# Optimization experiments

Hardware: AMD Instinct MI355X
Metric: run time of the kernel (lower is better)

## Reference

```python
import jax, jax.numpy as jnp
import numpy as np

N, E, F, H, L, G = 100000, 1600000, 32, 128, 4, 64


def gru_cell(m, h, w_ih, b_ih, w_hh, b_hh):
    # torch.nn.GRUCell math; gate order: r, z, n
    gi = m @ w_ih.T + b_ih          # [N, 3H]
    gh = h @ w_hh.T + b_hh          # [N, 3H]
    i_r, i_z, i_n = jnp.split(gi, 3, axis=-1)
    h_r, h_z, h_n = jnp.split(gh, 3, axis=-1)
    r = jax.nn.sigmoid(i_r + h_r)
    z = jax.nn.sigmoid(i_z + h_z)
    n = jnp.tanh(i_n + r * h_n)
    return (1.0 - z) * n + z * h


def setup_inputs() -> dict:
    key = jax.random.key(0)
    ks = jax.random.split(key, 12)
    s = 0.05
    return {
        "x": jax.random.normal(ks[0], (N, F), jnp.float32),
        "edge_index": jax.random.randint(ks[1], (2, E), 0, N, jnp.int64),
        "batch": jnp.sort(jax.random.randint(ks[2], (N,), 0, G, jnp.int64)),
        "num_graphs": G,
        "W0": jax.random.normal(ks[3], (H, F), jnp.float32) * s,
        "conv_w": jax.random.normal(ks[4], (L, H, H), jnp.float32) * s,
        "w_ih": jax.random.normal(ks[5], (3 * H, H), jnp.float32) * s,
        "b_ih": jax.random.normal(ks[6], (3 * H,), jnp.float32) * s,
        "w_hh": jax.random.normal(ks[7], (3 * H, H), jnp.float32) * s,
        "b_hh": jax.random.normal(ks[8], (3 * H,), jnp.float32) * s,
        "lin1_w": jax.random.normal(ks[9], (1, H), jnp.float32) * s,
        "lin1_b": jax.random.normal(ks[10], (1,), jnp.float32) * s,
    }


def reference(x, edge_index, batch, num_graphs, W0, conv_w, w_ih, b_ih, w_hh, b_hh, lin1_w, lin1_b):
    n_nodes = x.shape[0]
    # lin0 (no bias) + sigmoid embedding
    x_embed = jax.nn.sigmoid(x @ W0.T)                     # [N, H]

    src, dst = edge_index[0], edge_index[1]
    h = x_embed
    # GatedGraphConv: per layer, transform -> scatter-add over edges -> GRU update
    for l in range(conv_w.shape[0]):
        m = h @ conv_w[l]                                   # [N, H]
        agg = jax.ops.segment_sum(m[src], dst, num_segments=n_nodes)  # [N, H]
        h = gru_cell(agg, h, w_ih, b_ih, w_hh, b_hh)

    h = jax.nn.relu(h)
    out = h @ lin1_w.T + lin1_b                             # [N, 1]
    uncorrected = out

    # per-graph mean subtraction (scatter_mean + gather), same math as the loop
    sums = jax.ops.segment_sum(out, batch, num_segments=num_graphs)   # [G, 1]
    counts = jax.ops.segment_sum(jnp.ones((n_nodes, 1), out.dtype), batch, num_segments=num_graphs)
    mean_all = sums / jnp.maximum(counts, 1.0)
    corrected = out - mean_all[batch]

    return corrected.squeeze(1), x_embed, uncorrected.squeeze(1)
```

## Files before the change

### kernel.cpp

```cpp
#include <hip/hip_runtime.h>
#include <hip/hip_bf16.h>

#define HDIM 128
#define FDIM 32
#define GGR  64
#define SCAN_CHUNK 2048
#define FILL_CHUNK 1024
#define FILL_WIN 16

typedef __attribute__((ext_vector_type(8))) short bf16x8;
typedef __attribute__((ext_vector_type(4))) float f32x4;

__device__ __forceinline__ float fsig(float x) {
  return __builtin_amdgcn_rcpf(1.f + __expf(-x));
}
__device__ __forceinline__ float ftanh(float x) {
  return 1.f - 2.f * __builtin_amdgcn_rcpf(1.f + __expf(2.f * x));
}

__device__ __forceinline__ bf16x8 pack_bf16x8(float4 a, float4 b) {
  union { bf16x8 v; __hip_bfloat162 h[4]; } u;
  u.h[0] = __float22bfloat162_rn(make_float2(a.x, a.y));
  u.h[1] = __float22bfloat162_rn(make_float2(a.z, a.w));
  u.h[2] = __float22bfloat162_rn(make_float2(b.x, b.y));
  u.h[3] = __float22bfloat162_rn(make_float2(b.z, b.w));
  return u.v;
}

__device__ __forceinline__ int ablk(int kb, int m) {
  return (kb << 6) + (m & 56) + ((m ^ kb) & 7);
}

__device__ __forceinline__ void stage64(const unsigned short* __restrict__ g,
                                        short* __restrict__ s, int n0, int N, int t) {
#pragma unroll
  for (int r = 0; r < 2; ++r) {
    int idx = r * 512 + t;
    int m = idx >> 4, c8 = idx & 15;
    int gn = n0 + m;
    uint4 v = make_uint4(0u, 0u, 0u, 0u);
    if (gn < N) v = *(const uint4*)(g + (size_t)gn * HDIM + c8 * 8);
    *(uint4*)(s + ablk(c8, m) * 8) = v;
  }
}

__global__ __launch_bounds__(256) void k_embed_hist(const float* __restrict__ x,
                                                    const unsigned short* __restrict__ W0b,
                                                    unsigned short* __restrict__ hb,
                                                    float* __restrict__ xemb,
                                                    const unsigned short* __restrict__ convT0,
                                                    unsigned short* __restrict__ m_out,
                                                    int N,
                                                    const int* __restrict__ dst,
                                                    int* __restrict__ deg,
                                                    unsigned short* __restrict__ rank,
                                                    long long E, int histBlocks) {
  __shared__ short sE[16 * 64 * 8];
  if ((int)blockIdx.x < histBlocks) {
    long long e = (long long)blockIdx.x * 256 + threadIdx.x;
    if (e < E) {
      int old = atomicAdd(&deg[dst[e]], 1);
      rank[e] = (unsigned short)old;
    }
    return;
  }
  int bid = blockIdx.x - histBlocks;
  int t = threadIdx.x;
  int w = t >> 6, l = t & 63;
  int lm = l & 15, lq = l >> 4;
  int n0 = bid * 64;
  int j0 = w * 32;
  bf16x8 b0 = *(const bf16x8*)(W0b + (size_t)(j0 + lm) * FDIM + lq * 8);
  bf16x8 b1 = *(const bf16x8*)(W0b + (size_t)(j0 + 16 + lm) * FDIM + lq * 8);
  f32x4 acc0[4], acc1[4];
#pragma unroll
  for (int i = 0; i < 4; ++i) { acc0[i] = (f32x4){0.f,0.f,0.f,0.f}; acc1[i] = (f32x4){0.f,0.f,0.f,0.f}; }
#pragma unroll
  for (int tt = 0; tt < 4; ++tt) {
    int rg = n0 + tt * 16 + lm;
    bf16x8 a = (bf16x8){0,0,0,0,0,0,0,0};
    if (rg < N) {
      const float4* xr = (const float4*)x + (size_t)rg * 8 + lq * 2;
      a = pack_bf16x8(xr[0], xr[1]);
    }
    acc0[tt] = __builtin_amdgcn_mfma_f32_16x16x32_bf16(a, b0, acc0[tt], 0, 0, 0);
    acc1[tt] = __builtin_amdgcn_mfma_f32_16x16x32_bf16(a, b1, acc1[tt], 0, 0, 0);
  }
#pragma unroll
  for (int g = 0; g < 2; ++g) {
    int j = j0 + g * 16 + lm;
#pragma unroll
    for (int tt = 0; tt < 4; ++tt)
#pragma unroll
      for (int r = 0; r < 4; ++r) {
        int m = tt * 16 + lq * 4 + r;
        int node = n0 + m;
        float v = g ? acc1[tt][r] : acc0[tt][r];
        float e = fsig(v);
        __hip_bfloat16 eb = __float2bfloat16(e);
        ((__hip_bfloat16*)sE)[ablk(j >> 3, m) * 8 + (j & 7)] = eb;
        if (node < N) {
          size_t off = (size_t)node * HDIM + j;
          xemb[off] = e;
          ((__hip_bfloat16*)hb)[off] = eb;
        }
      }
  }
  __syncthreads();
#pragma unroll
  for (int g = 0; g < 2; ++g) {
    int jg = j0 + g * 16;
    f32x4 macc[4];
#pragma unroll
    for (int i = 0; i < 4; ++i) macc[i] = (f32x4){0.f,0.f,0.f,0.f};
#pragma unroll
    for (int ks = 0; ks < 4; ++ks) {
      bf16x8 b = *(const bf16x8*)(convT0 + (size_t)(jg + lm) * HDIM + ks * 32 + lq * 8);
      int kb = ks * 4 + lq;
#pragma unroll
      for (int tt = 0; tt < 4; ++tt) {
        bf16x8 a = *(const bf16x8*)(sE + ablk(kb, tt * 16 + lm) * 8);
        macc[tt] = __builtin_amdgcn_mfma_f32_16x16x32_bf16(a, b, macc[tt], 0, 0, 0);
      }
    }
    int j = jg + lm;
#pragma unroll
    for (int tt = 0; tt < 4; ++tt)
#pragma unroll
      for (int r = 0; r < 4; ++r) {
        int node = n0 + tt * 16 + lq * 4 + r;
        if (node < N)
          ((__hip_bfloat16*)m_out)[(size_t)node * HDIM + j] = __float2bfloat16(macc[tt][r]);
      }
  }
}

__global__ __launch_bounds__(256) void k_prep_w(const float* __restrict__ w_ih,
                                                const float* __restrict__ w_hh,
                                                const float* __restrict__ conv_w,
                                                const float* __restrict__ W0,
                                                unsigned short* __restrict__ wIb,
                                                unsigned short* __restrict__ wHb,
                                                unsigned short* __restrict__ convTb,
                                                unsigned short* __restrict__ W0b,
                                                int L) {
  int i = blockIdx.x * 256 + threadIdx.x;
  if (i < HDIM * FDIM) ((__hip_bfloat16*)W0b)[i] = __float2bfloat16(W0[i]);
  if (i < 384 * HDIM) {
    ((__hip_bfloat16*)wIb)[i] = __float2bfloat16(w_ih[i]);
    ((__hip_bfloat16*)wHb)[i] = __float2bfloat16(w_hh[i]);
  }
  int total = L * HDIM * HDIM;
  if (i < total) {
    int l = i >> 14, rem = i & 16383, j = rem >> 7, k = rem & 127;
    ((__hip_bfloat16*)convTb)[i] = __float2bfloat16(conv_w[(l << 14) + (k << 7) + j]);
  }
}

__global__ __launch_bounds__(256) void k_block_sum(const int* __restrict__ deg,
                                                   int* __restrict__ bsum, int N) {
  int base = blockIdx.x * SCAN_CHUNK + threadIdx.x * 8;
  int s = 0;
#pragma unroll
  for (int u = 0; u < 8; ++u) { int i = base + u; if (i < N) s += deg[i]; }
#pragma unroll
  for (int o = 32; o; o >>= 1) s += __shfl_down(s, o, 64);
  __shared__ int wsum[4];
  if ((threadIdx.x & 63) == 0) wsum[threadIdx.x >> 6] = s;
  __syncthreads();
  if (threadIdx.x == 0) bsum[blockIdx.x] = wsum[0] + wsum[1] + wsum[2] + wsum[3];
}

__global__ void k_scan_bsums(int* __restrict__ bsum, int nb) {
  if (blockIdx.x == 0 && threadIdx.x == 0) {
    int run = 0;
    for (int i = 0; i < nb; ++i) { int v = bsum[i]; bsum[i] = run; run += v; }
  }
}

__global__ __launch_bounds__(256) void k_scan_chunks(const int* __restrict__ deg,
                                                     const int* __restrict__ bsum,
                                                     int* __restrict__ rowstart,
                                                     int N, int Etot) {
  __shared__ int ts[256];
  int base = blockIdx.x * SCAN_CHUNK + threadIdx.x * 8;
  int loc[8]; int s = 0;
#pragma unroll
  for (int u = 0; u < 8; ++u) {
    int i = base + u; loc[u] = s;
    s += (i < N) ? deg[i] : 0;
  }
  ts[threadIdx.x] = s;
  __syncthreads();
  for (int o = 1; o < 256; o <<= 1) {
    int v = (threadIdx.x >= o) ? ts[threadIdx.x - o] : 0;
    __syncthreads();
    ts[threadIdx.x] += v;
    __syncthreads();
  }
  int texcl = (threadIdx.x ? ts[threadIdx.x - 1] : 0) + bsum[blockIdx.x];
#pragma unroll
  for (int u = 0; u < 8; ++u) {
    int i = base + u;
    if (i < N) rowstart[i] = texcl + loc[u];
  }
  if (blockIdx.x == 0 && threadIdx.x == 0) rowstart[N] = Etot;
}

__global__ __launch_bounds__(256) void k_csr_fill_win(const int* __restrict__ src,
                                                      const int* __restrict__ dst,
                                                      const unsigned short* __restrict__ rank,
                                                      const int* __restrict__ rowstart,
                                                      int* __restrict__ csr,
                                                      long long E, int N) {
  __shared__ int sd[FILL_CHUNK];
  __shared__ int ss[FILL_CHUNK];
  __shared__ unsigned short sr[FILL_CHUNK];
  long long base = (long long)blockIdx.x * FILL_CHUNK;
  int cnt = (int)((E - base < FILL_CHUNK) ? (E - base) : FILL_CHUNK);
  for (int i = threadIdx.x; i < cnt; i += 256) {
    sd[i] = dst[base + i];
    ss[i] = src[base + i];
    sr[i] = rank[base + i];
  }
  __syncthreads();
  int nw = (N + FILL_WIN - 1) / FILL_WIN;
#pragma unroll 1
  for (int w = 0; w < FILL_WIN; ++w) {
    int lo = w * nw, hi = lo + nw;
    for (int i = threadIdx.x; i < cnt; i += 256) {
      int d = sd[i];
      if (d >= lo && d < hi)
        csr[rowstart[d] + sr[i]] = ss[i];
    }
    __syncthreads();
  }
}

__global__ __launch_bounds__(256) void k_gather(const int* __restrict__ csr,
                                                const int* __restrict__ rowstart,
                                                const unsigned short* __restrict__ m,
                                                unsigned short* __restrict__ agg, int N) {
  int wv = threadIdx.x >> 6, l = threadIdx.x & 63;
  int n = blockIdx.x * 4 + wv;
  if (n >= N) return;
  int eq = l >> 3;
  int jb = l & 7;
  int beg = rowstart[n], end = rowstart[n + 1];
  float acc[16];
#pragma unroll
  for (int i = 0; i < 16; ++i) acc[i] = 0.f;
  for (int e0 = beg; e0 < end; e0 += 8) {
    int e = e0 + eq;
    uint4 v0 = make_uint4(0u, 0u, 0u, 0u);
    uint4 v1 = make_uint4(0u, 0u, 0u, 0u);
    if (e < end) {
      int s = csr[e];
      const uint4* row = (const uint4*)(m + (size_t)s * HDIM + jb * 16);
      v0 = row[0];
      v1 = row[1];
    }
    acc[0]  += __uint_as_float(v0.x << 16);
    acc[1]  += __uint_as_float(v0.x & 0xffff0000u);
    acc[2]  += __uint_as_float(v0.y << 16);
    acc[3]  += __uint_as_float(v0.y & 0xffff0000u);
    acc[4]  += __uint_as_float(v0.z << 16);
    acc[5]  += __uint_as_float(v0.z & 0xffff0000u);
    acc[6]  += __uint_as_float(v0.w << 16);
    acc[7]  += __uint_as_float(v0.w & 0xffff0000u);
    acc[8]  += __uint_as_float(v1.x << 16);
    acc[9]  += __uint_as_float(v1.x & 0xffff0000u);
    acc[10] += __uint_as_float(v1.y << 16);
    acc[11] += __uint_as_float(v1.y & 0xffff0000u);
    acc[12] += __uint_as_float(v1.z << 16);
    acc[13] += __uint_as_float(v1.z & 0xffff0000u);
    acc[14] += __uint_as_float(v1.w << 16);
    acc[15] += __uint_as_float(v1.w & 0xffff0000u);
  }
#pragma unroll
  for (int i = 0; i < 16; ++i) {
    acc[i] += __shfl_xor(acc[i], 8, 64);
    acc[i] += __shfl_xor(acc[i], 16, 64);
    acc[i] += __shfl_xor(acc[i], 32, 64);
  }
  if (eq == 0) {
    union { uint4 v[2]; __hip_bfloat162 h[8]; } o;
#pragma unroll
    for (int i = 0; i < 8; ++i)
      o.h[i] = __float22bfloat162_rn(make_float2(acc[2 * i], acc[2 * i + 1]));
    uint4* dstp = (uint4*)(agg + (size_t)n * HDIM + jb * 16);
    dstp[0] = o.v[0];
    dstp[1] = o.v[1];
  }
}

__global__ __launch_bounds__(512, 4) void k_gru_mfma(const unsigned short* __restrict__ aggb,
                                                  const unsigned short* __restrict__ hb,
                                                  const unsigned short* __restrict__ wI,
                                                  const unsigned short* __restrict__ wH,
                                                  const float* __restrict__ b_ih,
                                                  const float* __restrict__ b_hh,
                                                  unsigned short* __restrict__ hnewb,
                                                  const unsigned short* __restrict__ wT,
                                                  unsigned short* __restrict__ m_out,
                                                  int N) {
  __shared__ short sAg[16 * 64 * 8];
  __shared__ short sH[16 * 64 * 8];
  int t = threadIdx.x;
  int n0 = blockIdx.x * 64;
  stage64(aggb, sAg, n0, N, t);
  stage64(hb, sH, n0, N, t);
  int w = t >> 6, l = t & 63;
  int j0 = w * 16;
  int lm = l & 15, lq = l >> 4;
  int j = j0 + lm;
  float bir = b_ih[j], biz = b_ih[j + 128], bin = b_ih[j + 256];
  float bhr = b_hh[j], bhz = b_hh[j + 128], bhn = b_hh[j + 256];
  __syncthreads();
  f32x4 aR[4], aZ[4], aNi[4], aNh[4];
#pragma unroll
  for (int i = 0; i < 4; ++i) {
    aR[i] = (f32x4){0.f,0.f,0.f,0.f}; aZ[i] = (f32x4){0.f,0.f,0.f,0.f};
    aNi[i] = (f32x4){0.f,0.f,0.f,0.f}; aNh[i] = (f32x4){0.f,0.f,0.f,0.f};
  }
#pragma unroll
  for (int ks = 0; ks < 4; ++ks) {
    size_t rI = (size_t)(j0 + lm) * HDIM + ks * 32 + lq * 8;
    bf16x8 bIr = *(const bf16x8*)(wI + rI);
    bf16x8 bIz = *(const bf16x8*)(wI + rI + 128 * HDIM);
    bf16x8 bIn = *(const bf16x8*)(wI + rI + 256 * HDIM);
    bf16x8 bHr = *(const bf16x8*)(wH + rI);
    bf16x8 bHz = *(const bf16x8*)(wH + rI + 128 * HDIM);
    bf16x8 bHn = *(const bf16x8*)(wH + rI + 256 * HDIM);
    int kb = ks * 4 + lq;
#pragma unroll
    for (int tt = 0; tt < 4; ++tt) {
      bf16x8 a = *(const bf16x8*)(sAg + ablk(kb, tt * 16 + lm) * 8);
      bf16x8 h = *(const bf16x8*)(sH + ablk(kb, tt * 16 + lm) * 8);
      aR[tt] = __builtin_amdgcn_mfma_f32_16x16x32_bf16(a, bIr, aR[tt], 0, 0, 0);
      aR[tt] = __builtin_amdgcn_mfma_f32_16x16x32_bf16(h, bHr, aR[tt], 0, 0, 0);
      aZ[tt] = __builtin_amdgcn_mfma_f32_16x16x32_bf16(a, bIz, aZ[tt], 0, 0, 0);
      aZ[tt] = __builtin_amdgcn_mfma_f32_16x16x32_bf16(h, bHz, aZ[tt], 0, 0, 0);
      aNi[tt] = __builtin_amdgcn_mfma_f32_16x16x32_bf16(a, bIn, aNi[tt], 0, 0, 0);
      aNh[tt] = __builtin_amdgcn_mfma_f32_16x16x32_bf16(h, bHn, aNh[tt], 0, 0, 0);
    }
  }
  __syncthreads();
#pragma unroll
  for (int tt = 0; tt < 4; ++tt)
#pragma unroll
    for (int r = 0; r < 4; ++r) {
      int m = tt * 16 + lq * 4 + r;
      int node = n0 + m;
      float hp = __bfloat162float(((const __hip_bfloat16*)sH)[ablk(j >> 3, m) * 8 + (j & 7)]);
      float rg = fsig(aR[tt][r] + bir + bhr);
      float zg = fsig(aZ[tt][r] + biz + bhz);
      float nv = aNi[tt][r] + bin + rg * (aNh[tt][r] + bhn);
      float th = ftanh(nv);
      float hn = (1.f - zg) * th + zg * hp;
      __hip_bfloat16 hnb = __float2bfloat16(hn);
      ((__hip_bfloat16*)sAg)[ablk(j >> 3, m) * 8 + (j & 7)] = hnb;
      if (node < N)
        ((__hip_bfloat16*)hnewb)[(size_t)node * HDIM + j] = hnb;
    }
  if (wT) {
    __syncthreads();
    f32x4 macc[4];
#pragma unroll
    for (int i = 0; i < 4; ++i) macc[i] = (f32x4){0.f,0.f,0.f,0.f};
#pragma unroll
    for (int ks = 0; ks < 4; ++ks) {
      bf16x8 b = *(const bf16x8*)(wT + (size_t)(j0 + lm) * HDIM + ks * 32 + lq * 8);
      int kb = ks * 4 + lq;
#pragma unroll
      for (int tt = 0; tt < 4; ++tt) {
        bf16x8 a = *(const bf16x8*)(sAg + ablk(kb, tt * 16 + lm) * 8);
        macc[tt] = __builtin_amdgcn_mfma_f32_16x16x32_bf16(a, b, macc[tt], 0, 0, 0);
      }
    }
#pragma unroll
    for (int tt = 0; tt < 4; ++tt)
#pragma unroll
      for (int r = 0; r < 4; ++r) {
        int node = n0 + tt * 16 + lq * 4 + r;
        if (node < N)
          ((__hip_bfloat16*)m_out)[(size_t)node * HDIM + j] = __float2bfloat16(macc[tt][r]);
      }
  }
}

__global__ __launch_bounds__(256) void k_readout(const unsigned short* __restrict__ h,
                                                 const float* __restrict__ w1,
                                                 const float* __restrict__ b1,
                                                 float* __restrict__ out_raw,
                                                 float* __restrict__ uncorrected,
                                                 int N) {
  int wave = threadIdx.x >> 6;
  int lane = threadIdx.x & 63;
  int n = blockIdx.x * 4 + wave;
  if (n >= N) return;
  float h0 = __bfloat162float(((const __hip_bfloat16*)h)[(size_t)n * HDIM + lane]);
  float h1 = __bfloat162float(((const __hip_bfloat16*)h)[(size_t)n * HDIM + 64 + lane]);
  float v = fmaxf(h0, 0.f) * w1[lane] + fmaxf(h1, 0.f) * w1[64 + lane];
#pragma unroll
  for (int o = 32; o > 0; o >>= 1) v += __shfl_down(v, o, 64);
  if (lane == 0) {
    float o = v + b1[0];
    out_raw[n] = o;
    uncorrected[n] = o;
  }
}

__global__ __launch_bounds__(256) void k_graph_reduce(const float* __restrict__ out_raw,
                                                      const int* __restrict__ batch,
                                                      float* __restrict__ gsum,
                                                      float* __restrict__ gcnt,
                                                      int N) {
  __shared__ float ls[GGR], lc[GGR];
  int t = threadIdx.x;
  if (t < GGR) { ls[t] = 0.f; lc[t] = 0.f; }
  __syncthreads();
  for (int n = blockIdx.x * 256 + t; n < N; n += gridDim.x * 256) {
    int g = batch[n];
    atomicAdd(&ls[g], out_raw[n]);
    atomicAdd(&lc[g], 1.f);
  }
  __syncthreads();
  if (t < GGR) {
    unsafeAtomicAdd(&gsum[t], ls[t]);
    unsafeAtomicAdd(&gcnt[t], lc[t]);
  }
}

__global__ __launch_bounds__(256) void k_correct(const float* __restrict__ out_raw,
                                                 const int* __restrict__ batch,
                                                 const float* __restrict__ gsum,
                                                 const float* __restrict__ gcnt,
                                                 float* __restrict__ corrected, int N) {
  int n = blockIdx.x * 256 + threadIdx.x;
  if (n < N) {
    int g = batch[n];
    corrected[n] = out_raw[n] - gsum[g] / fmaxf(gcnt[g], 1.f);
  }
}

extern "C" void kernel_launch(void* const* d_in, const int* in_sizes, int n_in,
                              void* d_out, int out_size, void* d_ws, size_t ws_size,
                              hipStream_t stream) {
  const float* x      = (const float*)d_in[0];
  const int*   ei     = (const int*)d_in[1];
  const int*   batch  = (const int*)d_in[2];
  const float* W0     = (const float*)d_in[4];
  const float* conv_w = (const float*)d_in[5];
  const float* w_ih   = (const float*)d_in[6];
  const float* b_ih   = (const float*)d_in[7];
  const float* w_hh   = (const float*)d_in[8];
  const float* b_hh   = (const float*)d_in[9];
  const float* lin1_w = (const float*)d_in[10];
  const float* lin1_b = (const float*)d_in[11];

  int N = in_sizes[0] / FDIM;
  long long E = in_sizes[1] / 2;
  int L = in_sizes[5] / (HDIM * HDIM);

  const int* src = ei;
  const int* dstv = ei + E;

  float* out_corrected = (float*)d_out;
  float* out_xemb = out_corrected + N;
  float* out_unc  = out_xemb + (size_t)N * HDIM;

  char* p = (char*)d_ws;
  unsigned short* x0 = (unsigned short*)p; p += (size_t)N * HDIM * 2;
  unsigned short* x1 = (unsigned short*)p; p += (size_t)N * HDIM * 2;
  unsigned short* x2 = (unsigned short*)p; p += (size_t)N * HDIM * 2;
  float* out_raw = (float*)p;        p += (size_t)((N + 3) & ~3) * 4;
  float* gsum = (float*)p;           p += GGR * 4;
  float* gcnt = (float*)p;           p += GGR * 4;
  int* deg = (int*)p;                p += (size_t)((N + 3) & ~3) * 4;
  int* rowstart = (int*)p;           p += (size_t)(N + 4) * 4;
  int nb = (N + SCAN_CHUNK - 1) / SCAN_CHUNK;
  int* bsum = (int*)p;               p += (size_t)((nb + 63) & ~63) * 4;
  int* csr = (int*)p;                p += (size_t)E * 4;
  unsigned short* rankb = (unsigned short*)p;  p += (size_t)((E + 3) & ~3) * 2;
  unsigned short* wIb = (unsigned short*)p;    p += 384 * HDIM * 2;
  unsigned short* wHb = (unsigned short*)p;    p += 384 * HDIM * 2;
  unsigned short* convTb = (unsigned short*)p; p += (size_t)L * HDIM * HDIM * 2;
  unsigned short* W0b = (unsigned short*)p;

  int prep_total = (384 * HDIM > L * HDIM * HDIM) ? 384 * HDIM : L * HDIM * HDIM;
  k_prep_w<<<(prep_total + 255) / 256, 256, 0, stream>>>(w_ih, w_hh, conv_w, W0, wIb, wHb, convTb, W0b, L);

  hipMemsetAsync(deg, 0, (size_t)N * sizeof(int), stream);

  int nblk = (N + 63) / 64;
  int histBlocks = (int)((E + 255) / 256);
  k_embed_hist<<<histBlocks + nblk, 256, 0, stream>>>(x, W0b, x0, out_xemb, convTb, x1, N,
                                                      dstv, deg, rankb, E, histBlocks);

  k_block_sum<<<nb, 256, 0, stream>>>(deg, bsum, N);
  k_scan_bsums<<<1, 64, 0, stream>>>(bsum, nb);
  k_scan_chunks<<<nb, 256, 0, stream>>>(deg, bsum, rowstart, N, (int)E);
  k_csr_fill_win<<<(int)((E + FILL_CHUNK - 1) / FILL_CHUNK), 256, 0, stream>>>(
      src, dstv, rankb, rowstart, csr, E, N);

  unsigned short* Hb = x0;
  unsigned short* Mb = x1;
  for (int l = 0; l < L; ++l) {
    k_gather<<<(N + 3) / 4, 256, 0, stream>>>(csr, rowstart, Mb, x2, N);
    const unsigned short* wTn = (l + 1 < L) ? (convTb + (size_t)(l + 1) * HDIM * HDIM) : nullptr;
    k_gru_mfma<<<nblk, 512, 0, stream>>>(x2, Hb, wIb, wHb, b_ih, b_hh, Mb, wTn, Hb, N);
    unsigned short* tmp = Hb; Hb = Mb; Mb = tmp;
  }

  hipMemsetAsync(gsum, 0, 2 * GGR * sizeof(float), stream);
  k_readout<<<(N + 3) / 4, 256, 0, stream>>>(Hb, lin1_w, lin1_b, out_raw, out_unc, N);
  k_graph_reduce<<<256, 256, 0, stream>>>(out_raw, batch, gsum, gcnt, N);
  k_correct<<<(N + 255) / 256, 256, 0, stream>>>(out_raw, batch, gsum, gcnt, out_corrected, N);
}
```

Baseline: 740.7 us.

## Fuse CSR neighbor gather into GRU MFMA kernel via shared memory

Removes the separate gather kernel. Each GRU block now builds the aggregated messages for its 64 nodes directly in shared memory, one wave handling 8 nodes in turn. This drops the global write and re-read of the agg buffer plus one launch per layer. Buffers rotate across three arrays so the message input and the outputs never alias. The cost is lower parallelism for the latency-bound gather: 8 waves per block process nodes serially with fewer blocks in flight, and the GRU's occupancy limits now also apply to the gather.

```diff
diff --git a/kernel.cpp b/kernel.cpp
--- a/kernel.cpp
+++ b/kernel.cpp
@@ -237,64 +237,9 @@
   }
 }
 
-__global__ __launch_bounds__(256) void k_gather(const int* __restrict__ csr,
-                                                const int* __restrict__ rowstart,
-                                                const unsigned short* __restrict__ m,
-                                                unsigned short* __restrict__ agg, int N) {
-  int wv = threadIdx.x >> 6, l = threadIdx.x & 63;
-  int n = blockIdx.x * 4 + wv;
-  if (n >= N) return;
-  int eq = l >> 3;
-  int jb = l & 7;
-  int beg = rowstart[n], end = rowstart[n + 1];
-  float acc[16];
-#pragma unroll
-  for (int i = 0; i < 16; ++i) acc[i] = 0.f;
-  for (int e0 = beg; e0 < end; e0 += 8) {
-    int e = e0 + eq;
-    uint4 v0 = make_uint4(0u, 0u, 0u, 0u);
-    uint4 v1 = make_uint4(0u, 0u, 0u, 0u);
-    if (e < end) {
-      int s = csr[e];
-      const uint4* row = (const uint4*)(m + (size_t)s * HDIM + jb * 16);
-      v0 = row[0];
-      v1 = row[1];
-    }
-    acc[0]  += __uint_as_float(v0.x << 16);
-    acc[1]  += __uint_as_float(v0.x & 0xffff0000u);
-    acc[2]  += __uint_as_float(v0.y << 16);
-    acc[3]  += __uint_as_float(v0.y & 0xffff0000u);
-    acc[4]  += __uint_as_float(v0.z << 16);
-    acc[5]  += __uint_as_float(v0.z & 0xffff0000u);
-    acc[6]  += __uint_as_float(v0.w << 16);
-    acc[7]  += __uint_as_float(v0.w & 0xffff0000u);
-    acc[8]  += __uint_as_float(v1.x << 16);
-    acc[9]  += __uint_as_float(v1.x & 0xffff0000u);
-    acc[10] += __uint_as_float(v1.y << 16);
-    acc[11] += __uint_as_float(v1.y & 0xffff0000u);
-    acc[12] += __uint_as_float(v1.z << 16);
-    acc[13] += __uint_as_float(v1.z & 0xffff0000u);
-    acc[14] += __uint_as_float(v1.w << 16);
-    acc[15] += __uint_as_float(v1.w & 0xffff0000u);
-  }
-#pragma unroll
-  for (int i = 0; i < 16; ++i) {
-    acc[i] += __shfl_xor(acc[i], 8, 64);
-    acc[i] += __shfl_xor(acc[i], 16, 64);
-    acc[i] += __shfl_xor(acc[i], 32, 64);
-  }
-  if (eq == 0) {
-    union { uint4 v[2]; __hip_bfloat162 h[8]; } o;
-#pragma unroll
-    for (int i = 0; i < 8; ++i)
-      o.h[i] = __float22bfloat162_rn(make_float2(acc[2 * i], acc[2 * i + 1]));
-    uint4* dstp = (uint4*)(agg + (size_t)n * HDIM + jb * 16);
-    dstp[0] = o.v[0];
-    dstp[1] = o.v[1];
-  }
-}
-
-__global__ __launch_bounds__(512, 4) void k_gru_mfma(const unsigned short* __restrict__ aggb,
+__global__ __launch_bounds__(512, 4) void k_gru_mfma(const int* __restrict__ csr,
+                                                  const int* __restrict__ rowstart,
+                                                  const unsigned short* __restrict__ mb,
                                                   const unsigned short* __restrict__ hb,
                                                   const unsigned short* __restrict__ wI,
                                                   const unsigned short* __restrict__ wH,
@@ -308,7 +253,6 @@
   __shared__ short sH[16 * 64 * 8];
   int t = threadIdx.x;
   int n0 = blockIdx.x * 64;
-  stage64(aggb, sAg, n0, N, t);
   stage64(hb, sH, n0, N, t);
   int w = t >> 6, l = t & 63;
   int j0 = w * 16;
@@ -316,6 +260,62 @@
   int j = j0 + lm;
   float bir = b_ih[j], biz = b_ih[j + 128], bin = b_ih[j + 256];
   float bhr = b_hh[j], bhz = b_hh[j + 128], bhn = b_hh[j + 256];
+  {
+    int eq = l >> 3;
+    int jb = l & 7;
+#pragma unroll 1
+    for (int i = 0; i < 8; ++i) {
+      int m = w * 8 + i;
+      int n = n0 + m;
+      float acc[16];
+#pragma unroll
+      for (int k = 0; k < 16; ++k) acc[k] = 0.f;
+      if (n < N) {
+        int beg = rowstart[n], end = rowstart[n + 1];
+        for (int e0 = beg; e0 < end; e0 += 8) {
+          int e = e0 + eq;
+          uint4 v0 = make_uint4(0u, 0u, 0u, 0u);
+          uint4 v1 = make_uint4(0u, 0u, 0u, 0u);
+          if (e < end) {
+            int s = csr[e];
+            const uint4* row = (const uint4*)(mb + (size_t)s * HDIM + jb * 16);
+            v0 = row[0];
+            v1 = row[1];
+          }
+          acc[0]  += __uint_as_float(v0.x << 16);
+          acc[1]  += __uint_as_float(v0.x & 0xffff0000u);
+          acc[2]  += __uint_as_float(v0.y << 16);
+          acc[3]  += __uint_as_float(v0.y & 0xffff0000u);
+          acc[4]  += __uint_as_float(v0.z << 16);
+          acc[5]  += __uint_as_float(v0.z & 0xffff0000u);
+          acc[6]  += __uint_as_float(v0.w << 16);
+          acc[7]  += __uint_as_float(v0.w & 0xffff0000u);
+          acc[8]  += __uint_as_float(v1.x << 16);
+          acc[9]  += __uint_as_float(v1.x & 0xffff0000u);
+          acc[10] += __uint_as_float(v1.y << 16);
+          acc[11] += __uint_as_float(v1.y & 0xffff0000u);
+          acc[12] += __uint_as_float(v1.z << 16);
+          acc[13] += __uint_as_float(v1.z & 0xffff0000u);
+          acc[14] += __uint_as_float(v1.w << 16);
+          acc[15] += __uint_as_float(v1.w & 0xffff0000u);
+        }
+      }
+#pragma unroll
+      for (int k = 0; k < 16; ++k) {
+        acc[k] += __shfl_xor(acc[k], 8, 64);
+        acc[k] += __shfl_xor(acc[k], 16, 64);
+        acc[k] += __shfl_xor(acc[k], 32, 64);
+      }
+      if (eq == 0) {
+        union { uint4 v[2]; __hip_bfloat162 h[8]; } o;
+#pragma unroll
+        for (int k = 0; k < 8; ++k)
+          o.h[k] = __float22bfloat162_rn(make_float2(acc[2 * k], acc[2 * k + 1]));
+        *(uint4*)(sAg + ablk(2 * jb, m) * 8) = o.v[0];
+        *(uint4*)(sAg + ablk(2 * jb + 1, m) * 8) = o.v[1];
+      }
+    }
+  }
   __syncthreads();
   f32x4 aR[4], aZ[4], aNi[4], aNh[4];
 #pragma unroll
@@ -506,11 +506,14 @@
 
   unsigned short* Hb = x0;
   unsigned short* Mb = x1;
+  unsigned short* Fb = x2;
   for (int l = 0; l < L; ++l) {
-    k_gather<<<(N + 3) / 4, 256, 0, stream>>>(csr, rowstart, Mb, x2, N);
     const unsigned short* wTn = (l + 1 < L) ? (convTb + (size_t)(l + 1) * HDIM * HDIM) : nullptr;
-    k_gru_mfma<<<nblk, 512, 0, stream>>>(x2, Hb, wIb, wHb, b_ih, b_hh, Mb, wTn, Hb, N);
-    unsigned short* tmp = Hb; Hb = Mb; Mb = tmp;
+    k_gru_mfma<<<nblk, 512, 0, stream>>>(csr, rowstart, Mb, Hb, wIb, wHb, b_ih, b_hh,
+                                         Fb, wTn, Hb, N);
+    unsigned short* nH = Fb;
+    unsigned short* nM = Hb;
+    Fb = Mb; Hb = nH; Mb = nM;
   }
 
   hipMemsetAsync(gsum, 0, 2 * GGR * sizeof(float), stream);
```

After: 858.2 us. 15.9% more time.
